# Kernel optimization log

Hardware: AMD Instinct MI355X
Metric: run time of the kernel (lower is better)

The kernel has to match this reference:

```python
import jax, jax.numpy as jnp
import numpy as np

PRUNE_RATIO = 0.5
MIXUP_ALPHA = 0.05


def setup_inputs() -> dict:
    key = jax.random.key(0)
    k1, k2 = jax.random.split(key)
    seq = jax.random.normal(k1, (16, 4096, 1024), dtype=jnp.float32)
    attn_weights = jax.random.normal(k2, (16, 4096), dtype=jnp.float32)
    return {"seq": seq, "attn_weights": attn_weights}


def reference(seq, attn_weights):
    # Eval-mode forward (adversarial_mix only fires in training mode).
    B, N, D = seq.shape
    k = max(1, int(N * (1.0 - PRUNE_RATIO)))  # number of kept tokens
    _, top_idx = jax.lax.top_k(attn_weights, k)  # (B, k) int32
    # gather selected tokens: (B, k, D)
    selected = jnp.take_along_axis(seq, top_idx[:, :, None], axis=1)
    # mask of pruned (non-selected) tokens: ones scattered to zero at top_idx
    batch_ids = jnp.arange(B)[:, None]
    mask = jnp.ones((B, N), dtype=seq.dtype).at[batch_ids, top_idx].set(0.0)
    # masked mean of pruned tokens, scaled by mixup_alpha -> one extra token
    rem_sum = jnp.einsum('bn,bnd->bd', mask, seq)              # (B, D)
    rem_cnt = jnp.sum(mask, axis=1, keepdims=True) + 1e-10     # (B, 1)
    rem_tok = (MIXUP_ALPHA * rem_sum / rem_cnt)[:, None, :]    # (B, 1, D)
    return jnp.concatenate([selected, rem_tok], axis=1)         # (B, k+1, D)
```

## Files before the change

### kernel.cpp

```cpp
#include <hip/hip_runtime.h>

#define BATCH 16
#define NTOK  4096
#define DIM   1024
#define KSEL  2048
#define NPRUNE 2048
#define SLICES (NTOK / 256)
#define SUM_CHUNKS 64
#define ROWS_PER_CHUNK (NPRUNE / SUM_CHUNKS)
#define COPY_ROWS 4
#define NCOPY (KSEL / COPY_ROWS)

__global__ __launch_bounds__(256) void rank_kernel(
    const float* __restrict__ w, int* __restrict__ sel, int* __restrict__ pr) {
  __shared__ unsigned long long keys[NTOK];
  const int b = blockIdx.y;
  const float* wb = w + (size_t)b * NTOK;
  for (int j = threadIdx.x; j < NTOK; j += 256) {
    const unsigned int u = __float_as_uint(wb[j]);
    const unsigned int s = (u & 0x80000000u) ? ~u : (u | 0x80000000u);
    keys[j] = ((unsigned long long)(~s) << 32) | (unsigned int)j;
  }
  __syncthreads();

  const int i = blockIdx.x * 256 + threadIdx.x;
  const unsigned long long ki = keys[i];
  const ulonglong2* k2 = (const ulonglong2*)keys;
  unsigned int rank = 0;
#pragma unroll 8
  for (int j = 0; j < NTOK / 2; ++j) {
    const ulonglong2 kk = k2[j];
    rank += (kk.x < ki);
    rank += (kk.y < ki);
  }
  if (rank < KSEL) sel[b * KSEL + rank] = i;
  else             pr[b * NPRUNE + (rank - KSEL)] = i;
}

__global__ __launch_bounds__(256) void gather_partial_kernel(
    const float* __restrict__ seq, const int* __restrict__ sel,
    const int* __restrict__ pr, float* __restrict__ out,
    float* __restrict__ part) {
  const int b = blockIdx.y;
  const int t = blockIdx.x;
  const float4* seqb = (const float4*)(seq + (size_t)b * NTOK * DIM);
  const int lane = threadIdx.x;

  if (t < SUM_CHUNKS) {
    const int* prb = pr + b * NPRUNE + t * ROWS_PER_CHUNK;
    float4 a0 = make_float4(0.f, 0.f, 0.f, 0.f), a1 = a0, a2 = a0, a3 = a0;
    for (int r = 0; r < ROWS_PER_CHUNK; r += 4) {
      const int r0 = prb[r + 0], r1 = prb[r + 1];
      const int r2 = prb[r + 2], r3 = prb[r + 3];
      const float4 x0 = seqb[(size_t)r0 * (DIM / 4) + lane];
      const float4 x1 = seqb[(size_t)r1 * (DIM / 4) + lane];
      const float4 x2 = seqb[(size_t)r2 * (DIM / 4) + lane];
      const float4 x3 = seqb[(size_t)r3 * (DIM / 4) + lane];
      a0.x += x0.x; a0.y += x0.y; a0.z += x0.z; a0.w += x0.w;
      a1.x += x1.x; a1.y += x1.y; a1.z += x1.z; a1.w += x1.w;
      a2.x += x2.x; a2.y += x2.y; a2.z += x2.z; a2.w += x2.w;
      a3.x += x3.x; a3.y += x3.y; a3.z += x3.z; a3.w += x3.w;
    }
    float4 acc;
    acc.x = (a0.x + a1.x) + (a2.x + a3.x);
    acc.y = (a0.y + a1.y) + (a2.y + a3.y);
    acc.z = (a0.z + a1.z) + (a2.z + a3.z);
    acc.w = (a0.w + a1.w) + (a2.w + a3.w);
    float4* pdst = (float4*)(part + ((size_t)b * SUM_CHUNKS + t) * DIM);
    pdst[lane] = acc;
  } else {
    const int c = t - SUM_CHUNKS;
    const int base = c * COPY_ROWS;
    const int* selb = sel + b * KSEL + base;
    const int i0 = selb[0], i1 = selb[1], i2 = selb[2], i3 = selb[3];
    const float4 x0 = seqb[(size_t)i0 * (DIM / 4) + lane];
    const float4 x1 = seqb[(size_t)i1 * (DIM / 4) + lane];
    const float4 x2 = seqb[(size_t)i2 * (DIM / 4) + lane];
    const float4 x3 = seqb[(size_t)i3 * (DIM / 4) + lane];
    float4* dst = (float4*)(out + (size_t)b * (KSEL + 1) * DIM +
                            (size_t)base * DIM);
    dst[0 * (DIM / 4) + lane] = x0;
    dst[1 * (DIM / 4) + lane] = x1;
    dst[2 * (DIM / 4) + lane] = x2;
    dst[3 * (DIM / 4) + lane] = x3;
  }
}

__global__ __launch_bounds__(256) void reduce_kernel(
    const float* __restrict__ part, float* __restrict__ out, float scale) {
  const int b = blockIdx.x;
  const float4* p = (const float4*)(part + (size_t)b * SUM_CHUNKS * DIM);
  float4 acc = make_float4(0.f, 0.f, 0.f, 0.f);
  for (int c = 0; c < SUM_CHUNKS; ++c) {
    const float4 x = p[(size_t)c * (DIM / 4) + threadIdx.x];
    acc.x += x.x; acc.y += x.y; acc.z += x.z; acc.w += x.w;
  }
  float4* dst = (float4*)(out + (size_t)b * (KSEL + 1) * DIM +
                          (size_t)KSEL * DIM);
  float4 r;
  r.x = acc.x * scale; r.y = acc.y * scale;
  r.z = acc.z * scale; r.w = acc.w * scale;
  dst[threadIdx.x] = r;
}

extern "C" void kernel_launch(void* const* d_in, const int* in_sizes, int n_in,
                              void* d_out, int out_size, void* d_ws, size_t ws_size,
                              hipStream_t stream) {
  (void)in_sizes; (void)n_in; (void)out_size; (void)ws_size;
  const float* seq = (const float*)d_in[0];
  const float* w   = (const float*)d_in[1];
  float* out = (float*)d_out;

  int* sel = (int*)d_ws;
  int* pr  = sel + BATCH * KSEL;
  float* part = (float*)(pr + BATCH * NPRUNE);

  rank_kernel<<<dim3(SLICES, BATCH), 256, 0, stream>>>(w, sel, pr);
  gather_partial_kernel<<<dim3(SUM_CHUNKS + NCOPY, BATCH), 256, 0, stream>>>(
      seq, sel, pr, out, part);
  const float scale = (float)(0.05 / (2048.0 + 1e-10));
  reduce_kernel<<<BATCH, 256, 0, stream>>>(part, out, scale);
}
```

Before: 453.0 us.

## Replace O(N^2) rank sort with histogram bucket ranking, add nontemporal gathers

The all-pairs rank kernel, which compares every token key against all 4096 keys, is replaced by a one-block-per-batch histogram approach. Keys are binned on their top 12 bits, a prefix scan gives bucket offsets, keys are scattered into buckets, and each token's rank is resolved by comparing only within its own bucket. The gather/partial-sum kernel now uses nontemporal vector loads and stores, and the final reduce is split across four blocks per batch with a shared-memory combine. The new rank kernel runs only 16 blocks and its cost depends on the bucket distribution. With normally distributed weights, buckets with many keys could serialise the within-bucket loop.

```diff
diff --git a/kernel.cpp b/kernel.cpp
--- a/kernel.cpp
+++ b/kernel.cpp
@@ -5,36 +5,95 @@
 #define DIM   1024
 #define KSEL  2048
 #define NPRUNE 2048
-#define SLICES (NTOK / 256)
 #define SUM_CHUNKS 64
 #define ROWS_PER_CHUNK (NPRUNE / SUM_CHUNKS)
 #define COPY_ROWS 4
 #define NCOPY (KSEL / COPY_ROWS)
 
-__global__ __launch_bounds__(256) void rank_kernel(
+#define NBIN 4096
+#define RTHREADS 1024
+#define TPT (NTOK / RTHREADS)
+#define BPT (NBIN / RTHREADS)
+
+typedef __attribute__((ext_vector_type(4))) float f32x4;
+
+__global__ __launch_bounds__(1024) void rank_kernel(
     const float* __restrict__ w, int* __restrict__ sel, int* __restrict__ pr) {
-  __shared__ unsigned long long keys[NTOK];
-  const int b = blockIdx.y;
+  __shared__ unsigned int s_cnt[NBIN];
+  __shared__ unsigned int s_base[NBIN];
+  __shared__ unsigned int s_cur[NBIN];
+  __shared__ unsigned long long s_key[NTOK];
+  __shared__ unsigned int s_wsum[16];
+  __shared__ unsigned int s_woff[16];
+
+  const int b = blockIdx.x;
+  const int t = threadIdx.x;
   const float* wb = w + (size_t)b * NTOK;
-  for (int j = threadIdx.x; j < NTOK; j += 256) {
+
+  for (int i = t; i < NBIN; i += RTHREADS) s_cnt[i] = 0;
+  __syncthreads();
+
+  unsigned int inv[TPT];
+  unsigned int bin[TPT];
+  int tok[TPT];
+#pragma unroll
+  for (int p = 0; p < TPT; ++p) {
+    const int j = p * RTHREADS + t;
     const unsigned int u = __float_as_uint(wb[j]);
     const unsigned int s = (u & 0x80000000u) ? ~u : (u | 0x80000000u);
-    keys[j] = ((unsigned long long)(~s) << 32) | (unsigned int)j;
+    const unsigned int iv = ~s;
+    inv[p] = iv; tok[p] = j; bin[p] = iv >> 20;
+    atomicAdd(&s_cnt[bin[p]], 1u);
   }
   __syncthreads();
 
-  const int i = blockIdx.x * 256 + threadIdx.x;
-  const unsigned long long ki = keys[i];
-  const ulonglong2* k2 = (const ulonglong2*)keys;
-  unsigned int rank = 0;
-#pragma unroll 8
-  for (int j = 0; j < NTOK / 2; ++j) {
-    const ulonglong2 kk = k2[j];
-    rank += (kk.x < ki);
-    rank += (kk.y < ki);
+  unsigned int c[BPT];
+  unsigned int lsum = 0;
+#pragma unroll
+  for (int i = 0; i < BPT; ++i) { c[i] = s_cnt[t * BPT + i]; lsum += c[i]; }
+  const int lane = t & 63, wid = t >> 6;
+  unsigned int v = lsum;
+  for (int d = 1; d < 64; d <<= 1) {
+    unsigned int up = __shfl_up(v, d, 64);
+    if (lane >= d) v += up;
   }
-  if (rank < KSEL) sel[b * KSEL + rank] = i;
-  else             pr[b * NPRUNE + (rank - KSEL)] = i;
+  if (lane == 63) s_wsum[wid] = v;
+  __syncthreads();
+  if (t == 0) {
+    unsigned int run = 0;
+    for (int i = 0; i < 16; ++i) { const unsigned int x = s_wsum[i]; s_woff[i] = run; run += x; }
+  }
+  __syncthreads();
+  unsigned int excl = v - lsum + s_woff[wid];
+#pragma unroll
+  for (int i = 0; i < BPT; ++i) {
+    s_base[t * BPT + i] = excl;
+    s_cur[t * BPT + i] = excl;
+    excl += c[i];
+  }
+  __syncthreads();
+
+  unsigned long long key[TPT];
+#pragma unroll
+  for (int p = 0; p < TPT; ++p) {
+    key[p] = ((unsigned long long)inv[p] << 32) | (unsigned int)tok[p];
+    const unsigned int pos = atomicAdd(&s_cur[bin[p]], 1u);
+    s_key[pos] = key[p];
+  }
+  __syncthreads();
+
+  int* selb = sel + b * KSEL;
+  int* prb  = pr + b * NPRUNE;
+#pragma unroll
+  for (int p = 0; p < TPT; ++p) {
+    const unsigned int bb = bin[p];
+    const unsigned int st = s_base[bb];
+    const unsigned int en = s_cur[bb];
+    unsigned int r = st;
+    for (unsigned int q = st; q < en; ++q) r += (s_key[q] < key[p]);
+    if (r < KSEL) selb[r] = tok[p];
+    else          prb[r - KSEL] = tok[p];
+  }
 }
 
 __global__ __launch_bounds__(256) void gather_partial_kernel(
@@ -43,64 +102,65 @@
     float* __restrict__ part) {
   const int b = blockIdx.y;
   const int t = blockIdx.x;
-  const float4* seqb = (const float4*)(seq + (size_t)b * NTOK * DIM);
+  const f32x4* seqb = (const f32x4*)(seq + (size_t)b * NTOK * DIM);
   const int lane = threadIdx.x;
 
   if (t < SUM_CHUNKS) {
     const int* prb = pr + b * NPRUNE + t * ROWS_PER_CHUNK;
-    float4 a0 = make_float4(0.f, 0.f, 0.f, 0.f), a1 = a0, a2 = a0, a3 = a0;
+    f32x4 a0 = {0.f, 0.f, 0.f, 0.f}, a1 = a0, a2 = a0, a3 = a0;
+#pragma unroll
     for (int r = 0; r < ROWS_PER_CHUNK; r += 4) {
       const int r0 = prb[r + 0], r1 = prb[r + 1];
       const int r2 = prb[r + 2], r3 = prb[r + 3];
-      const float4 x0 = seqb[(size_t)r0 * (DIM / 4) + lane];
-      const float4 x1 = seqb[(size_t)r1 * (DIM / 4) + lane];
-      const float4 x2 = seqb[(size_t)r2 * (DIM / 4) + lane];
-      const float4 x3 = seqb[(size_t)r3 * (DIM / 4) + lane];
-      a0.x += x0.x; a0.y += x0.y; a0.z += x0.z; a0.w += x0.w;
-      a1.x += x1.x; a1.y += x1.y; a1.z += x1.z; a1.w += x1.w;
-      a2.x += x2.x; a2.y += x2.y; a2.z += x2.z; a2.w += x2.w;
-      a3.x += x3.x; a3.y += x3.y; a3.z += x3.z; a3.w += x3.w;
+      const f32x4 x0 = __builtin_nontemporal_load(seqb + (size_t)r0 * (DIM / 4) + lane);
+      const f32x4 x1 = __builtin_nontemporal_load(seqb + (size_t)r1 * (DIM / 4) + lane);
+      const f32x4 x2 = __builtin_nontemporal_load(seqb + (size_t)r2 * (DIM / 4) + lane);
+      const f32x4 x3 = __builtin_nontemporal_load(seqb + (size_t)r3 * (DIM / 4) + lane);
+      a0 += x0; a1 += x1; a2 += x2; a3 += x3;
     }
-    float4 acc;
-    acc.x = (a0.x + a1.x) + (a2.x + a3.x);
-    acc.y = (a0.y + a1.y) + (a2.y + a3.y);
-    acc.z = (a0.z + a1.z) + (a2.z + a3.z);
-    acc.w = (a0.w + a1.w) + (a2.w + a3.w);
-    float4* pdst = (float4*)(part + ((size_t)b * SUM_CHUNKS + t) * DIM);
+    const f32x4 acc = (a0 + a1) + (a2 + a3);
+    f32x4* pdst = (f32x4*)(part + ((size_t)b * SUM_CHUNKS + t) * DIM);
     pdst[lane] = acc;
   } else {
     const int c = t - SUM_CHUNKS;
     const int base = c * COPY_ROWS;
     const int* selb = sel + b * KSEL + base;
     const int i0 = selb[0], i1 = selb[1], i2 = selb[2], i3 = selb[3];
-    const float4 x0 = seqb[(size_t)i0 * (DIM / 4) + lane];
-    const float4 x1 = seqb[(size_t)i1 * (DIM / 4) + lane];
-    const float4 x2 = seqb[(size_t)i2 * (DIM / 4) + lane];
-    const float4 x3 = seqb[(size_t)i3 * (DIM / 4) + lane];
-    float4* dst = (float4*)(out + (size_t)b * (KSEL + 1) * DIM +
-                            (size_t)base * DIM);
-    dst[0 * (DIM / 4) + lane] = x0;
-    dst[1 * (DIM / 4) + lane] = x1;
-    dst[2 * (DIM / 4) + lane] = x2;
-    dst[3 * (DIM / 4) + lane] = x3;
+    const f32x4 x0 = __builtin_nontemporal_load(seqb + (size_t)i0 * (DIM / 4) + lane);
+    const f32x4 x1 = __builtin_nontemporal_load(seqb + (size_t)i1 * (DIM / 4) + lane);
+    const f32x4 x2 = __builtin_nontemporal_load(seqb + (size_t)i2 * (DIM / 4) + lane);
+    const f32x4 x3 = __builtin_nontemporal_load(seqb + (size_t)i3 * (DIM / 4) + lane);
+    f32x4* dst = (f32x4*)(out + (size_t)b * (KSEL + 1) * DIM +
+                          (size_t)base * DIM);
+    __builtin_nontemporal_store(x0, dst + 0 * (DIM / 4) + lane);
+    __builtin_nontemporal_store(x1, dst + 1 * (DIM / 4) + lane);
+    __builtin_nontemporal_store(x2, dst + 2 * (DIM / 4) + lane);
+    __builtin_nontemporal_store(x3, dst + 3 * (DIM / 4) + lane);
   }
 }
 
 __global__ __launch_bounds__(256) void reduce_kernel(
     const float* __restrict__ part, float* __restrict__ out, float scale) {
-  const int b = blockIdx.x;
-  const float4* p = (const float4*)(part + (size_t)b * SUM_CHUNKS * DIM);
-  float4 acc = make_float4(0.f, 0.f, 0.f, 0.f);
-  for (int c = 0; c < SUM_CHUNKS; ++c) {
-    const float4 x = p[(size_t)c * (DIM / 4) + threadIdx.x];
-    acc.x += x.x; acc.y += x.y; acc.z += x.z; acc.w += x.w;
+  __shared__ f32x4 s_acc[4][64];
+  const int b = blockIdx.y, qq = blockIdx.x;
+  const int t = threadIdx.x, g = t >> 6, col = t & 63;
+  const int c4 = qq * 64 + col;
+  const f32x4* p = (const f32x4*)(part + (size_t)b * SUM_CHUNKS * DIM);
+  f32x4 acc = {0.f, 0.f, 0.f, 0.f};
+#pragma unroll
+  for (int i = 0; i < SUM_CHUNKS / 4; ++i) {
+    const int ch = g + 4 * i;
+    acc += p[(size_t)ch * (DIM / 4) + c4];
   }
-  float4* dst = (float4*)(out + (size_t)b * (KSEL + 1) * DIM +
+  s_acc[g][col] = acc;
+  __syncthreads();
+  if (g == 0) {
+    f32x4 r = (s_acc[0][col] + s_acc[1][col]) + (s_acc[2][col] + s_acc[3][col]);
+    r *= scale;
+    f32x4* dst = (f32x4*)(out + (size_t)b * (KSEL + 1) * DIM +
                           (size_t)KSEL * DIM);
-  float4 r;
-  r.x = acc.x * scale; r.y = acc.y * scale;
-  r.z = acc.z * scale; r.w = acc.w * scale;
-  dst[threadIdx.x] = r;
+    dst[c4] = r;
+  }
 }
 
 extern "C" void kernel_launch(void* const* d_in, const int* in_sizes, int n_in,
@@ -115,9 +175,9 @@
   int* pr  = sel + BATCH * KSEL;
   float* part = (float*)(pr + BATCH * NPRUNE);
 
-  rank_kernel<<<dim3(SLICES, BATCH), 256, 0, stream>>>(w, sel, pr);
+  rank_kernel<<<BATCH, RTHREADS, 0, stream>>>(w, sel, pr);
   gather_partial_kernel<<<dim3(SUM_CHUNKS + NCOPY, BATCH), 256, 0, stream>>>(
       seq, sel, pr, out, part);
   const float scale = (float)(0.05 / (2048.0 + 1e-10));
-  reduce_kernel<<<BATCH, 256, 0, stream>>>(part, out, scale);
+  reduce_kernel<<<dim3(4, BATCH), 256, 0, stream>>>(part, out, scale);
 }
```

Result: faster. 414.8 us (-8.4%).
